# Kernel optimization log

Measured on AMD Instinct MI355X. Metric: run time of the kernel, lower is better.

## Reference

```python
import jax, jax.numpy as jnp
import numpy as np

HEADS = 8
DIM_HEAD = 64
DIM = 512
B, N = 4, 2048
SCALE = DIM_HEAD ** -0.5


def setup_inputs() -> dict:
    key = jax.random.key(0)
    k1, k2, k3, k4, k5, k6 = jax.random.split(key, 6)
    inner = HEADS * DIM_HEAD
    s = DIM ** -0.5
    return {
        "input_feature": jax.random.normal(k1, (B, N, DIM), dtype=jnp.float32),
        "mask": jax.random.randint(k2, (B, N), 0, 2, dtype=jnp.int32),
        "Wq": jax.random.normal(k3, (inner, DIM), dtype=jnp.float32) * s,
        "Wk": jax.random.normal(k4, (inner, DIM), dtype=jnp.float32) * s,
        "Wv": jax.random.normal(k5, (inner, DIM), dtype=jnp.float32) * s,
        "Wout": jax.random.normal(k6, (DIM, inner), dtype=jnp.float32) * s,
    }


def reference(input_feature, mask, Wq, Wk, Wv, Wout):
    # Conv1d with kernel_size=1, no bias == per-token linear: out = W @ x_channels
    q = jnp.einsum('bnc,dc->bnd', input_feature, Wq)  # [B, N, H*Dh]
    k = jnp.einsum('bnc,dc->bnd', input_feature, Wk)
    v = jnp.einsum('bnc,dc->bnd', input_feature, Wv)

    # '(n c)' channel layout is head-major -> reshape to [B, N, H, Dh], move head out front
    def split_heads(t):
        return t.reshape(B, N, HEADS, DIM_HEAD).transpose(2, 0, 1, 3)  # [H, B, N, Dh]

    q, k, v = split_heads(q), split_heads(k), split_heads(v)

    scores = jnp.einsum('hbtd,hbsd->hbts', q, k) * SCALE  # [H, B, N, N]
    # masked_fill(mask == 0, 1e-9): fill with small CONSTANT (not -inf), faithful to source
    m = (mask == 0)[None, :, None, :]  # [1, B, 1, N]
    scores = jnp.where(m, jnp.float32(1e-9), scores)
    att = jax.nn.softmax(scores, axis=-1)
    out = jnp.einsum('hbts,hbsd->hbtd', att, v)  # [H, B, N, Dh]

    # '(n b) tokens c -> b (n c) tokens' : head-major channel concat
    out = out.transpose(1, 2, 0, 3).reshape(B, N, HEADS * DIM_HEAD)  # [B, N, H*Dh]
    out = jnp.einsum('bnd,ed->bne', out, Wout)  # [B, N, DIM]
    return out
```

## Files before the change

### kernel.cpp

```cpp
#include <hip/hip_runtime.h>
#include <hip/hip_bf16.h>

typedef __attribute__((ext_vector_type(8))) short short8;
typedef __attribute__((ext_vector_type(4))) short short4_t;
typedef __attribute__((ext_vector_type(4))) float float4_;

#define LOG2E 1.4426950408889634f

__device__ __forceinline__ short f2bf(float f) {
    unsigned int u = __builtin_bit_cast(unsigned int, f);
    u = (u + 0x7FFFu + ((u >> 16) & 1u)) >> 16;
    return (short)u;
}

__device__ __forceinline__ unsigned pk2bf(float a, float b) {
    unsigned ua = __builtin_bit_cast(unsigned, a) + 0x8000u;
    unsigned ub = __builtin_bit_cast(unsigned, b) + 0x8000u;
    return __builtin_amdgcn_perm(ub, ua, 0x07060302);
}

__device__ __forceinline__ void gload_lds16(const short* g, short* l) {
    __builtin_amdgcn_global_load_lds((const __attribute__((address_space(1))) void*)g,
                                     (__attribute__((address_space(3))) void*)l, 16, 0, 0);
}

__global__ __launch_bounds__(256) void cvt_kernel(
    const float* __restrict__ X, const float* __restrict__ Wq, const float* __restrict__ Wk,
    const float* __restrict__ Wv, const float* __restrict__ Wo,
    short* __restrict__ Xb, short* __restrict__ Wqkb, short* __restrict__ Wvb, short* __restrict__ Wob) {
    int i = blockIdx.x * 256 + threadIdx.x;
    const float* src; short* dst; float sc = 1.0f;
    if (i < 1048576) { src = X + (size_t)i * 4; dst = Xb + (size_t)i * 4; }
    else {
        int w = i - 1048576; int sec = w >> 16; int j = (w & 65535) * 4;
        if (sec == 0)      { src = Wq + j; dst = Wqkb + j; sc = 0.125f * LOG2E; }
        else if (sec == 1) { src = Wk + j; dst = Wqkb + 262144 + j; }
        else if (sec == 2) { src = Wv + j; dst = Wvb + j; }
        else               { src = Wo + j; dst = Wob + j; }
    }
    float4 v = *(const float4*)src;
    short4_t o;
    o[0] = f2bf(v.x * sc); o[1] = f2bf(v.y * sc); o[2] = f2bf(v.z * sc); o[3] = f2bf(v.w * sc);
    *(short4_t*)dst = o;
}

template<int MODE>
__global__ __launch_bounds__(256) void gemm_bt(const short* __restrict__ A, const short* __restrict__ B,
                                               void* __restrict__ C, short* __restrict__ C2,
                                               const int* __restrict__ mask) {
    __shared__ short At[128 * 32];
    __shared__ short Bt[128 * 32];
    constexpr int K = 512;
    int tid = threadIdx.x;
    int wid = tid >> 6, lane = tid & 63;
    int quad = lane >> 4, cc = lane & 15;
    int wr = wid >> 1, wc = wid & 1;
    int m0 = blockIdx.y * 128, n0 = blockIdx.x * 128;
    const short* Ag = A;
    const short* Bg = (MODE == 1) ? (B + (size_t)blockIdx.z * 2048 * 512) : B;

    float4_ acc[4][4] = {};

    for (int kk = 0; kk < K; kk += 32) {
#pragma unroll
        for (int i = 0; i < 2; ++i) {
            int lb = wid * 1024 + i * 4096 + lane * 16;
            int row = lb >> 6;
            int ke = (lb & 63) >> 1;
            gload_lds16(Ag + (size_t)(m0 + row) * K + kk + ke, At + (lb >> 1));
            gload_lds16(Bg + (size_t)(n0 + row) * K + kk + ke, Bt + (lb >> 1));
        }
        __syncthreads();
        short8 af[4], bf[4];
#pragma unroll
        for (int i = 0; i < 4; ++i) af[i] = *(const short8*)(At + (wr * 64 + i * 16 + cc) * 32 + quad * 8);
#pragma unroll
        for (int j = 0; j < 4; ++j) bf[j] = *(const short8*)(Bt + (wc * 64 + j * 16 + cc) * 32 + quad * 8);
#pragma unroll
        for (int i = 0; i < 4; ++i)
#pragma unroll
            for (int j = 0; j < 4; ++j)
                acc[i][j] = __builtin_amdgcn_mfma_f32_16x16x32_bf16(af[i], bf[j], acc[i][j], 0, 0, 0);
        __syncthreads();
    }

#pragma unroll
    for (int i = 0; i < 4; ++i) {
#pragma unroll
        for (int j = 0; j < 4; ++j) {
#pragma unroll
            for (int r = 0; r < 4; ++r) {
                int gm = m0 + wr * 64 + i * 16 + quad * 4 + r;
                int gn = n0 + wc * 64 + j * 16 + cc;
                float v = acc[i][j][r];
                if (MODE == 0) {
                    int which = gn >> 9;
                    int hd = gn & 511;
                    int h = hd >> 6, dh = hd & 63;
                    int b = gm >> 11, nn = gm & 2047;
                    if (which && mask[gm] == 0) v = 0.0f;
                    short* dst = (which ? C2 : (short*)C);
                    dst[((((size_t)b * 8 + h) * 2048 + nn) * 64) + dh] = f2bf(v);
                } else if (MODE == 1) {
                    ((short*)C)[(size_t)blockIdx.z * 512 * 2048 + (size_t)gm * 2048 + gn] = f2bf(v);
                } else {
                    ((float*)C)[(size_t)gm * 512 + gn] = v;
                }
            }
        }
    }
}

__global__ __launch_bounds__(256) void attn_kernel(const short* __restrict__ Q, const short* __restrict__ Kg,
                                                   const short* __restrict__ Vt,
                                                   short* __restrict__ AO) {
    __shared__ __align__(16) char smem[40960];
    short* KbufL = (short*)smem;
    short* VbufL = (short*)(smem + 16384);
    short* Pt    = (short*)(smem + 32768);
    float* Lw    = (float*)smem;
    float* Lfin  = (float*)(smem + 1024);

    int tid = threadIdx.x;
    int w = tid >> 6, lane = tid & 63;
    int quad = lane >> 4, cc = lane & 15;
    int tg = w >> 1, dh = w & 1;
    int bh = blockIdx.x, b = bh >> 3, h = bh & 7;
    int t0 = blockIdx.y * 64;
    size_t kbase = (size_t)bh * 2048 * 64;
    size_t vbase = (size_t)b * 512 * 2048 + (size_t)h * 64 * 2048;

    short8 qf[4][2];
#pragma unroll
    for (int tb = 0; tb < 4; ++tb)
#pragma unroll
        for (int kc = 0; kc < 2; ++kc)
            qf[tb][kc] = *(const short8*)(Q + kbase + (size_t)(t0 + tb * 16 + cc) * 64 + kc * 32 + quad * 8);

    int c7 = cc & 7;
    int koff[2], poff_w[4], aoff[2][2], voff[2][2];
#pragma unroll
    for (int kc = 0; kc < 2; ++kc)
        koff[kc] = (w * 16 + cc) * 64 + (((kc * 4 + quad) ^ c7) * 8);
#pragma unroll
    for (int tb = 0; tb < 4; ++tb)
        poff_w[tb] = (tb * 16 + cc) * 64 + (((w * 2 + (quad >> 1)) ^ c7) * 8) + (quad & 1) * 4;
#pragma unroll
    for (int mb = 0; mb < 2; ++mb)
#pragma unroll
        for (int kc = 0; kc < 2; ++kc)
            aoff[mb][kc] = (tg * 32 + mb * 16 + cc) * 64 + (((kc * 4 + quad) ^ c7) * 8);
#pragma unroll
    for (int db = 0; db < 2; ++db)
#pragma unroll
        for (int kc = 0; kc < 2; ++kc)
            voff[db][kc] = (dh * 32 + db * 16 + cc) * 64 + (((kc * 4 + quad) ^ c7) * 8);

    float4_ o[2][2] = {};
    float lp[4] = {0.f, 0.f, 0.f, 0.f};

#pragma unroll
    for (int pass = 0; pass < 4; ++pass) {
        int slot = pass * 256 + tid;
        if (slot < 512) {
            int s = slot >> 3, c = slot & 7;
            gload_lds16(Kg + kbase + (size_t)s * 64 + ((c ^ (s & 7)) * 8), KbufL + slot * 8);
        } else {
            int q = slot - 512;
            int d = q >> 3, c = q & 7;
            gload_lds16(Vt + vbase + (size_t)d * 2048 + ((c ^ (d & 7)) * 8), VbufL + q * 8);
        }
    }

    for (int it = 0; it < 32; ++it) {
        int cur = it & 1;
        const short* Kt  = KbufL + cur * 4096;
        const short* Vtt = VbufL + cur * 4096;
        __syncthreads();

        if (it < 31) {
            int s1 = (it + 1) * 64;
            short* Kn = KbufL + (cur ^ 1) * 4096;
            short* Vn = VbufL + (cur ^ 1) * 4096;
#pragma unroll
            for (int pass = 0; pass < 4; ++pass) {
                int slot = pass * 256 + tid;
                if (slot < 512) {
                    int s = slot >> 3, c = slot & 7;
                    gload_lds16(Kg + kbase + (size_t)(s1 + s) * 64 + ((c ^ (s & 7)) * 8), Kn + slot * 8);
                } else {
                    int q = slot - 512;
                    int d = q >> 3, c = q & 7;
                    gload_lds16(Vt + vbase + (size_t)d * 2048 + s1 + ((c ^ (d & 7)) * 8), Vn + q * 8);
                }
            }
        }

        short8 kf0 = *(const short8*)(Kt + koff[0]);
        short8 kf1 = *(const short8*)(Kt + koff[1]);
        float4_ acc[4];
#pragma unroll
        for (int tb = 0; tb < 4; ++tb) {
            float4_ a = {0.f, 0.f, 0.f, 0.f};
            a = __builtin_amdgcn_mfma_f32_16x16x32_bf16(kf0, qf[tb][0], a, 0, 0, 0);
            a = __builtin_amdgcn_mfma_f32_16x16x32_bf16(kf1, qf[tb][1], a, 0, 0, 0);
            acc[tb] = a;
        }
#pragma unroll
        for (int tb = 0; tb < 4; ++tb) {
            float x0 = __builtin_amdgcn_exp2f(acc[tb][0]);
            float x1 = __builtin_amdgcn_exp2f(acc[tb][1]);
            float x2 = __builtin_amdgcn_exp2f(acc[tb][2]);
            float x3 = __builtin_amdgcn_exp2f(acc[tb][3]);
            lp[tb] += (x0 + x1) + (x2 + x3);
            uint2 pw; pw.x = pk2bf(x0, x1); pw.y = pk2bf(x2, x3);
            *(uint2*)(Pt + poff_w[tb]) = pw;
        }
        __syncthreads();

        short8 af[2][2], vf[2][2];
#pragma unroll
        for (int mb = 0; mb < 2; ++mb)
#pragma unroll
            for (int kc = 0; kc < 2; ++kc)
                af[mb][kc] = *(const short8*)(Pt + aoff[mb][kc]);
#pragma unroll
        for (int db = 0; db < 2; ++db)
#pragma unroll
            for (int kc = 0; kc < 2; ++kc)
                vf[db][kc] = *(const short8*)(Vtt + voff[db][kc]);
#pragma unroll
        for (int mb = 0; mb < 2; ++mb)
#pragma unroll
            for (int db = 0; db < 2; ++db) {
                o[mb][db] = __builtin_amdgcn_mfma_f32_16x16x32_bf16(af[mb][0], vf[db][0], o[mb][db], 0, 0, 0);
                o[mb][db] = __builtin_amdgcn_mfma_f32_16x16x32_bf16(af[mb][1], vf[db][1], o[mb][db], 0, 0, 0);
            }
    }

#pragma unroll
    for (int tb = 0; tb < 4; ++tb) {
        lp[tb] += __shfl_xor(lp[tb], 16, 64);
        lp[tb] += __shfl_xor(lp[tb], 32, 64);
    }
    __syncthreads();
    if (lane < 16) {
#pragma unroll
        for (int tb = 0; tb < 4; ++tb) Lw[w * 64 + tb * 16 + lane] = lp[tb];
    }
    __syncthreads();
    if (tid < 64) {
        float s = Lw[tid] + Lw[64 + tid] + Lw[128 + tid] + Lw[192 + tid];
        Lfin[tid] = 1.0f / s;
    }
    __syncthreads();

#pragma unroll
    for (int mb = 0; mb < 2; ++mb)
#pragma unroll
        for (int r = 0; r < 4; ++r) {
            int tl = tg * 32 + mb * 16 + quad * 4 + r;
            float inv = Lfin[tl];
            size_t rowbase = ((size_t)(b * 2048 + t0 + tl)) * 512 + h * 64;
#pragma unroll
            for (int db = 0; db < 2; ++db)
                AO[rowbase + dh * 32 + db * 16 + cc] = f2bf(o[mb][db][r] * inv);
        }
}

extern "C" void kernel_launch(void* const* d_in, const int* in_sizes, int n_in,
                              void* d_out, int out_size, void* d_ws, size_t ws_size,
                              hipStream_t stream) {
    const float* X  = (const float*)d_in[0];
    const int* mask = (const int*)d_in[1];
    const float* Wq = (const float*)d_in[2];
    const float* Wk = (const float*)d_in[3];
    const float* Wv = (const float*)d_in[4];
    const float* Wo = (const float*)d_in[5];

    char* ws = (char*)d_ws;
    short* Xbf  = (short*)(ws + 0);
    short* Wqkb = (short*)(ws + 8388608);
    short* Wvb  = (short*)(ws + 9437184);
    short* Wob  = (short*)(ws + 9961472);
    short* Qb   = (short*)(ws + 10485760);
    short* Kb   = (short*)(ws + 18874368);
    short* Vtb  = (short*)(ws + 27262976);
    short* AOb  = (short*)(ws + 35651584);

    cvt_kernel<<<5120, 256, 0, stream>>>(X, Wq, Wk, Wv, Wo, Xbf, Wqkb, Wvb, Wob);
    gemm_bt<0><<<dim3(8, 64, 1), 256, 0, stream>>>(Xbf, Wqkb, (void*)Qb, Kb, mask);
    gemm_bt<1><<<dim3(16, 4, 4), 256, 0, stream>>>(Wvb, Xbf, (void*)Vtb, nullptr, nullptr);
    attn_kernel<<<dim3(32, 32), 256, 0, stream>>>(Qb, Kb, Vtb, AOb);
    gemm_bt<2><<<dim3(4, 64, 1), 256, 0, stream>>>(AOb, Wob, d_out, nullptr, nullptr);
}
```

Baseline: 190.8 us.

## Fuse Q/K/V projections into one GEMM and shrink output GEMM tiles

Merges the separate V-transpose GEMM into the Q/K projection GEMM by concatenating Wq/Wk/Wv into one weight buffer, so one launch of 768 blocks writes Q, K and transposed V. V is stored with packed 4-wide writes along the token dimension, and the mask is staged once per block in shared memory. The output projection gets its own kernel with 64-row tiles, which doubles its block count for better occupancy. This removes one launch and a second pass over X, at the cost of a divergent epilogue per block.

```diff
diff --git a/kernel.cpp b/kernel.cpp
--- a/kernel.cpp
+++ b/kernel.cpp
@@ -27,15 +27,15 @@
 __global__ __launch_bounds__(256) void cvt_kernel(
     const float* __restrict__ X, const float* __restrict__ Wq, const float* __restrict__ Wk,
     const float* __restrict__ Wv, const float* __restrict__ Wo,
-    short* __restrict__ Xb, short* __restrict__ Wqkb, short* __restrict__ Wvb, short* __restrict__ Wob) {
+    short* __restrict__ Xb, short* __restrict__ Wqkvb, short* __restrict__ Wob) {
     int i = blockIdx.x * 256 + threadIdx.x;
     const float* src; short* dst; float sc = 1.0f;
     if (i < 1048576) { src = X + (size_t)i * 4; dst = Xb + (size_t)i * 4; }
     else {
         int w = i - 1048576; int sec = w >> 16; int j = (w & 65535) * 4;
-        if (sec == 0)      { src = Wq + j; dst = Wqkb + j; sc = 0.125f * LOG2E; }
-        else if (sec == 1) { src = Wk + j; dst = Wqkb + 262144 + j; }
-        else if (sec == 2) { src = Wv + j; dst = Wvb + j; }
+        if (sec == 0)      { src = Wq + j; dst = Wqkvb + j; sc = 0.125f * LOG2E; }
+        else if (sec == 1) { src = Wk + j; dst = Wqkvb + 262144 + j; }
+        else if (sec == 2) { src = Wv + j; dst = Wqkvb + 524288 + j; }
         else               { src = Wo + j; dst = Wob + j; }
     }
     float4 v = *(const float4*)src;
@@ -44,20 +44,20 @@
     *(short4_t*)dst = o;
 }
 
-template<int MODE>
-__global__ __launch_bounds__(256) void gemm_bt(const short* __restrict__ A, const short* __restrict__ B,
-                                               void* __restrict__ C, short* __restrict__ C2,
-                                               const int* __restrict__ mask) {
+__global__ __launch_bounds__(256) void gemm_qkv(const short* __restrict__ A, const short* __restrict__ B,
+                                                const int* __restrict__ mask,
+                                                short* __restrict__ Qb, short* __restrict__ Kb,
+                                                short* __restrict__ Vtb) {
     __shared__ short At[128 * 32];
     __shared__ short Bt[128 * 32];
+    __shared__ int maskL[128];
     constexpr int K = 512;
     int tid = threadIdx.x;
     int wid = tid >> 6, lane = tid & 63;
     int quad = lane >> 4, cc = lane & 15;
     int wr = wid >> 1, wc = wid & 1;
     int m0 = blockIdx.y * 128, n0 = blockIdx.x * 128;
-    const short* Ag = A;
-    const short* Bg = (MODE == 1) ? (B + (size_t)blockIdx.z * 2048 * 512) : B;
+    if (tid < 128) maskL[tid] = mask[m0 + tid];
 
     float4_ acc[4][4] = {};
 
@@ -67,8 +67,8 @@
             int lb = wid * 1024 + i * 4096 + lane * 16;
             int row = lb >> 6;
             int ke = (lb & 63) >> 1;
-            gload_lds16(Ag + (size_t)(m0 + row) * K + kk + ke, At + (lb >> 1));
-            gload_lds16(Bg + (size_t)(n0 + row) * K + kk + ke, Bt + (lb >> 1));
+            gload_lds16(A + (size_t)(m0 + row) * K + kk + ke, At + (lb >> 1));
+            gload_lds16(B + (size_t)(n0 + row) * K + kk + ke, Bt + (lb >> 1));
         }
         __syncthreads();
         short8 af[4], bf[4];
@@ -84,27 +84,36 @@
         __syncthreads();
     }
 
-#pragma unroll
-    for (int i = 0; i < 4; ++i) {
-#pragma unroll
-        for (int j = 0; j < 4; ++j) {
-#pragma unroll
-            for (int r = 0; r < 4; ++r) {
-                int gm = m0 + wr * 64 + i * 16 + quad * 4 + r;
-                int gn = n0 + wc * 64 + j * 16 + cc;
-                float v = acc[i][j][r];
-                if (MODE == 0) {
-                    int which = gn >> 9;
-                    int hd = gn & 511;
+    int which = n0 >> 9;
+    int b = m0 >> 11;
+    if (which == 2) {
+#pragma unroll
+        for (int i = 0; i < 4; ++i) {
+#pragma unroll
+            for (int j = 0; j < 4; ++j) {
+                int d = (n0 & 511) + wc * 64 + j * 16 + cc;
+                int nn = (m0 & 2047) + wr * 64 + i * 16 + quad * 4;
+                short4_t pv;
+                pv[0] = f2bf(acc[i][j][0]); pv[1] = f2bf(acc[i][j][1]);
+                pv[2] = f2bf(acc[i][j][2]); pv[3] = f2bf(acc[i][j][3]);
+                *(short4_t*)(Vtb + ((size_t)(b * 512 + d)) * 2048 + nn) = pv;
+            }
+        }
+    } else {
+        short* dst = which ? Kb : Qb;
+#pragma unroll
+        for (int i = 0; i < 4; ++i) {
+#pragma unroll
+            for (int j = 0; j < 4; ++j) {
+#pragma unroll
+                for (int r = 0; r < 4; ++r) {
+                    int lm = wr * 64 + i * 16 + quad * 4 + r;
+                    int nn = (m0 & 2047) + lm;
+                    int hd = (n0 & 511) + wc * 64 + j * 16 + cc;
                     int h = hd >> 6, dh = hd & 63;
-                    int b = gm >> 11, nn = gm & 2047;
-                    if (which && mask[gm] == 0) v = 0.0f;
-                    short* dst = (which ? C2 : (short*)C);
+                    float v = acc[i][j][r];
+                    if (which == 1 && maskL[lm] == 0) v = 0.0f;
                     dst[((((size_t)b * 8 + h) * 2048 + nn) * 64) + dh] = f2bf(v);
-                } else if (MODE == 1) {
-                    ((short*)C)[(size_t)blockIdx.z * 512 * 2048 + (size_t)gm * 2048 + gn] = f2bf(v);
-                } else {
-                    ((float*)C)[(size_t)gm * 512 + gn] = v;
                 }
             }
         }
@@ -268,6 +277,53 @@
         }
 }
 
+__global__ __launch_bounds__(256) void gemm_out(const short* __restrict__ A, const short* __restrict__ B,
+                                                float* __restrict__ C) {
+    __shared__ short At[64 * 32];
+    __shared__ short Bt[128 * 32];
+    constexpr int K = 512;
+    int tid = threadIdx.x;
+    int wid = tid >> 6, lane = tid & 63;
+    int quad = lane >> 4, cc = lane & 15;
+    int wr = wid >> 1, wc = wid & 1;
+    int m0 = blockIdx.y * 64, n0 = blockIdx.x * 128;
+
+    float4_ acc[2][4] = {};
+
+    for (int kk = 0; kk < K; kk += 32) {
+        {
+            int row = tid >> 2, ke = (tid & 3) * 8;
+            gload_lds16(A + (size_t)(m0 + row) * K + kk + ke, At + tid * 8);
+            gload_lds16(B + (size_t)(n0 + row) * K + kk + ke, Bt + tid * 8);
+            int row2 = (tid + 256) >> 2;
+            gload_lds16(B + (size_t)(n0 + row2) * K + kk + ke, Bt + tid * 8 + 2048);
+        }
+        __syncthreads();
+        short8 af[2], bf[4];
+#pragma unroll
+        for (int i = 0; i < 2; ++i) af[i] = *(const short8*)(At + (wr * 32 + i * 16 + cc) * 32 + quad * 8);
+#pragma unroll
+        for (int j = 0; j < 4; ++j) bf[j] = *(const short8*)(Bt + (wc * 64 + j * 16 + cc) * 32 + quad * 8);
+#pragma unroll
+        for (int i = 0; i < 2; ++i)
+#pragma unroll
+            for (int j = 0; j < 4; ++j)
+                acc[i][j] = __builtin_amdgcn_mfma_f32_16x16x32_bf16(af[i], bf[j], acc[i][j], 0, 0, 0);
+        __syncthreads();
+    }
+
+#pragma unroll
+    for (int i = 0; i < 2; ++i)
+#pragma unroll
+        for (int j = 0; j < 4; ++j)
+#pragma unroll
+            for (int r = 0; r < 4; ++r) {
+                int gm = m0 + wr * 32 + i * 16 + quad * 4 + r;
+                int gn = n0 + wc * 64 + j * 16 + cc;
+                C[(size_t)gm * 512 + gn] = acc[i][j][r];
+            }
+}
+
 extern "C" void kernel_launch(void* const* d_in, const int* in_sizes, int n_in,
                               void* d_out, int out_size, void* d_ws, size_t ws_size,
                               hipStream_t stream) {
@@ -279,18 +335,16 @@
     const float* Wo = (const float*)d_in[5];
 
     char* ws = (char*)d_ws;
-    short* Xbf  = (short*)(ws + 0);
-    short* Wqkb = (short*)(ws + 8388608);
-    short* Wvb  = (short*)(ws + 9437184);
-    short* Wob  = (short*)(ws + 9961472);
-    short* Qb   = (short*)(ws + 10485760);
-    short* Kb   = (short*)(ws + 18874368);
-    short* Vtb  = (short*)(ws + 27262976);
-    short* AOb  = (short*)(ws + 35651584);
-
-    cvt_kernel<<<5120, 256, 0, stream>>>(X, Wq, Wk, Wv, Wo, Xbf, Wqkb, Wvb, Wob);
-    gemm_bt<0><<<dim3(8, 64, 1), 256, 0, stream>>>(Xbf, Wqkb, (void*)Qb, Kb, mask);
-    gemm_bt<1><<<dim3(16, 4, 4), 256, 0, stream>>>(Wvb, Xbf, (void*)Vtb, nullptr, nullptr);
+    short* Xbf   = (short*)(ws + 0);
+    short* Wqkvb = (short*)(ws + 8388608);
+    short* Wob   = (short*)(ws + 9961472);
+    short* Qb    = (short*)(ws + 10485760);
+    short* Kb    = (short*)(ws + 18874368);
+    short* Vtb   = (short*)(ws + 27262976);
+    short* AOb   = (short*)(ws + 35651584);
+
+    cvt_kernel<<<5120, 256, 0, stream>>>(X, Wq, Wk, Wv, Wo, Xbf, Wqkvb, Wob);
+    gemm_qkv<<<dim3(12, 64), 256, 0, stream>>>(Xbf, Wqkvb, mask, Qb, Kb, Vtb);
     attn_kernel<<<dim3(32, 32), 256, 0, stream>>>(Qb, Kb, Vtb, AOb);
-    gemm_bt<2><<<dim3(4, 64, 1), 256, 0, stream>>>(AOb, Wob, d_out, nullptr, nullptr);
-}
+    gemm_out<<<dim3(4, 128), 256, 0, stream>>>(AOb, Wob, (float*)d_out);
+}
```

After: 175.5 us. 8.0% less time.
